# Kernel tuning notes

Hardware: AMD Instinct MI355X
Metric: run time of the kernel (lower is better)

## Reference

```python
import jax, jax.numpy as jnp
import numpy as np

B, D, H = 8192, 256, 64


def setup_inputs() -> dict:
    key = jax.random.key(0)
    ks = jax.random.split(key, 7)
    noise = jax.random.normal(ks[0], (B, D), dtype=jnp.float32)
    adj_logits = jax.random.normal(ks[1], (D, D), dtype=jnp.float32) * 0.1
    # stacked per-node mechanism params: Linear(D,H) -> SiLU -> Linear(H,1)
    W1 = jax.random.normal(ks[2], (D, H, D), dtype=jnp.float32) * (1.0 / np.sqrt(D))
    b1 = jax.random.normal(ks[3], (D, H), dtype=jnp.float32) * (1.0 / np.sqrt(D))
    W2 = jax.random.normal(ks[4], (D, H), dtype=jnp.float32) * (1.0 / np.sqrt(H))
    b2 = jax.random.normal(ks[5], (D,), dtype=jnp.float32) * (1.0 / np.sqrt(H))
    log_sigma = jnp.zeros((D,), dtype=jnp.float32)  # torch init: tensor(0.0)
    return {"noise": noise, "adj_logits": adj_logits, "W1": W1, "b1": b1,
            "W2": W2, "b2": b2, "log_sigma": log_sigma}


def reference(noise, adj_logits, W1, b1, W2, b2, log_sigma):
    d = adj_logits.shape[0]
    # differentiable adjacency: sigmoid(logits) with zeroed diagonal
    adj = jax.nn.sigmoid(adj_logits) * (1.0 - jnp.eye(d, dtype=adj_logits.dtype))
    bsz = noise.shape[0]
    z0 = jnp.zeros((bsz, d), dtype=noise.dtype)

    def step(z, xs):
        i, a_col, w1, bb1, w2, bb2, ls, n_i = xs
        pv = z * a_col[None, :]                       # [B, D] masked parent values
        h = jax.nn.silu(pv @ w1.T + bb1[None, :])     # [B, H]
        det = h @ w2 + bb2                            # [B]
        val = det + jnp.exp(ls) * n_i                 # [B]
        z = jax.lax.dynamic_update_slice(z, val[:, None], (0, i))
        return z, None

    xs = (jnp.arange(d), adj.T, W1, b1, W2, b2, log_sigma, noise.T)
    z, _ = jax.lax.scan(step, z0, xs)
    return z
```

## Files before the change

kernel.cpp:

```cpp
#include <hip/hip_runtime.h>
#include <math.h>

#define Dn 256
#define Hn 64
#define BT 32

typedef __attribute__((ext_vector_type(8))) short short8;
typedef float floatx4 __attribute__((ext_vector_type(4)));

static __device__ __forceinline__ unsigned short f2bf(float x) {
    unsigned int u = __float_as_uint(x);
    unsigned int r = (u + 0x7fffu + ((u >> 16) & 1u)) >> 16;
    return (unsigned short)r;
}

__global__ __launch_bounds__(256) void prep_wb(const float* __restrict__ W1,
                                               const float* __restrict__ adj,
                                               unsigned short* __restrict__ Wb) {
    const int c = blockIdx.x, i = blockIdx.y;
    const int t = threadIdx.x;
    const int w = t >> 6, l = t & 63;
    const int kk = w * 16 + (l & 15);
    const int jb = c * 32 + ((l >> 4) & 3) * 8;
    const float* wp = W1 + ((size_t)i * Hn + kk) * Dn + jb;
    unsigned short v[8];
#pragma unroll
    for (int e = 0; e < 8; ++e) {
        int j = jb + e;
        float m = 0.f;
        if (j != i) m = 1.f / (1.f + __expf(-adj[(size_t)j * Dn + i]));
        v[e] = f2bf(wp[e] * m);
    }
    unsigned short* dst = Wb + ((((size_t)i * 8 + c) * 4 + w) * 64 + l) * 8;
    *(short8*)dst = *(const short8*)v;
}

__global__ __launch_bounds__(256, 1) void scm_main(const unsigned short* __restrict__ Wb,
                                                   const float* __restrict__ b1,
                                                   const float* __restrict__ W2,
                                                   const float* __restrict__ b2,
                                                   const float* __restrict__ log_sigma,
                                                   const float* __restrict__ noise,
                                                   float* __restrict__ out) {
    __shared__ unsigned short zbf[BT][264];
    __shared__ float ns[BT][257];
    __shared__ float part[4][34];
    __shared__ float sgv[Dn];
    __shared__ float b2v[Dn];

    const int t = threadIdx.x;
    const int w = t >> 6;
    const int l = t & 63;
    const int n = l & 15;
    const int q = l >> 4;
    const size_t rowbase = (size_t)blockIdx.x * BT;

    for (int idx = t; idx < BT * 264; idx += 256) (&zbf[0][0])[idx] = 0;
    {
        const float4* np4 = (const float4*)noise;
        for (int idx = t; idx < BT * (Dn / 4); idx += 256) {
            int r = idx >> 6, jq = idx & 63;
            float4 v = np4[(rowbase + r) * (Dn / 4) + jq];
            ns[r][jq * 4 + 0] = v.x; ns[r][jq * 4 + 1] = v.y;
            ns[r][jq * 4 + 2] = v.z; ns[r][jq * 4 + 3] = v.w;
        }
    }
    sgv[t] = __expf(log_sigma[t]);
    b2v[t] = b2[t];
    __syncthreads();

    short8 af0[8], af1[8];
#pragma unroll
    for (int c = 0; c < 8; ++c) { af0[c] = (short8)0; af1[c] = (short8)0; }

    const int kk = w * 16 + n;
    const unsigned short* wb_l = Wb + (size_t)w * 512 + (size_t)l * 8;

    for (int i = 0; i < Dn; ++i) {
        const int cc = (i + 31) >> 5;
        const int lc = (i - 1) >> 5;

        float b1v = b1[i * Hn + kk];
        float w2v = W2[i * Hn + kk];

        short8 bf[8];
        const unsigned short* wrow = wb_l + (size_t)i * 16384;
#pragma unroll
        for (int c = 0; c < 8; ++c)
            if (c < cc) bf[c] = *(const short8*)(wrow + (size_t)c * 2048);

        if (i >= 1) {
#pragma unroll
            for (int c = 0; c < 8; ++c)
                if (c == lc) {
                    af0[c] = *(const short8*)&zbf[n][c * 32 + q * 8];
                    af1[c] = *(const short8*)&zbf[16 + n][c * 32 + q * 8];
                }
        }

        floatx4 acc0 = {0.f, 0.f, 0.f, 0.f};
        floatx4 acc1 = {0.f, 0.f, 0.f, 0.f};
#pragma unroll
        for (int c = 0; c < 8; ++c)
            if (c < cc) {
                acc0 = __builtin_amdgcn_mfma_f32_16x16x32_bf16(af0[c], bf[c], acc0, 0, 0, 0);
                acc1 = __builtin_amdgcn_mfma_f32_16x16x32_bf16(af1[c], bf[c], acc1, 0, 0, 0);
            }

        float d0[4], d1[4];
#pragma unroll
        for (int r = 0; r < 4; ++r) {
            float h0 = acc0[r] + b1v;
            float h1 = acc1[r] + b1v;
            d0[r] = __fdividef(h0, 1.f + __expf(-h0)) * w2v;
            d1[r] = __fdividef(h1, 1.f + __expf(-h1)) * w2v;
        }
#pragma unroll
        for (int m = 1; m <= 8; m <<= 1) {
#pragma unroll
            for (int r = 0; r < 4; ++r) {
                d0[r] += __shfl_xor(d0[r], m);
                d1[r] += __shfl_xor(d1[r], m);
            }
        }
        if (n == 0) {
#pragma unroll
            for (int r = 0; r < 4; ++r) {
                part[w][q * 4 + r]      = d0[r];
                part[w][16 + q * 4 + r] = d1[r];
            }
        }
        __syncthreads();
        if (t < BT) {
            int r = t;
            float z = part[0][r] + part[1][r] + part[2][r] + part[3][r]
                    + b2v[i] + sgv[i] * ns[r][i];
            zbf[r][i] = f2bf(z);
            out[(rowbase + r) * Dn + i] = z;
        }
        __syncthreads();
    }
}

extern "C" void kernel_launch(void* const* d_in, const int* in_sizes, int n_in,
                              void* d_out, int out_size, void* d_ws, size_t ws_size,
                              hipStream_t stream) {
    const float* noise      = (const float*)d_in[0];
    const float* adj_logits = (const float*)d_in[1];
    const float* W1         = (const float*)d_in[2];
    const float* b1         = (const float*)d_in[3];
    const float* W2         = (const float*)d_in[4];
    const float* b2         = (const float*)d_in[5];
    const float* log_sigma  = (const float*)d_in[6];
    float* out = (float*)d_out;

    const int B = in_sizes[0] / Dn;
    unsigned short* Wb = (unsigned short*)d_ws;

    dim3 g1(8, Dn);
    prep_wb<<<g1, 256, 0, stream>>>(W1, adj_logits, Wb);

    dim3 g2(B / BT);
    scm_main<<<g2, 256, 0, stream>>>(Wb, b1, W2, b2, log_sigma, noise, out);
}
```

Baseline: 424.7 us.

## Make each wave own 16 rows and remove block barriers from the sequential scan

```diff
diff --git a/kernel.cpp b/kernel.cpp
--- a/kernel.cpp
+++ b/kernel.cpp
@@ -3,7 +3,6 @@
 
 #define Dn 256
 #define Hn 64
-#define BT 32
 
 typedef __attribute__((ext_vector_type(8))) short short8;
 typedef float floatx4 __attribute__((ext_vector_type(4)));
@@ -14,131 +13,175 @@
     return (unsigned short)r;
 }
 
+__global__ __launch_bounds__(256) void prep_sgm(const float* __restrict__ adj,
+                                                float* __restrict__ sgm) {
+    const int i = blockIdx.x, j = threadIdx.x;
+    float m = 0.f;
+    if (j != i) m = 1.f / (1.f + __expf(-adj[(size_t)j * Dn + i]));
+    sgm[(size_t)i * Dn + j] = m;
+}
+
 __global__ __launch_bounds__(256) void prep_wb(const float* __restrict__ W1,
-                                               const float* __restrict__ adj,
+                                               const float* __restrict__ sgm,
                                                unsigned short* __restrict__ Wb) {
     const int c = blockIdx.x, i = blockIdx.y;
     const int t = threadIdx.x;
-    const int w = t >> 6, l = t & 63;
-    const int kk = w * 16 + (l & 15);
+    const int nb = t >> 6, l = t & 63;
+    const int kk = nb * 16 + (l & 15);
     const int jb = c * 32 + ((l >> 4) & 3) * 8;
     const float* wp = W1 + ((size_t)i * Hn + kk) * Dn + jb;
+    const float* sp = sgm + (size_t)i * Dn + jb;
     unsigned short v[8];
 #pragma unroll
-    for (int e = 0; e < 8; ++e) {
-        int j = jb + e;
-        float m = 0.f;
-        if (j != i) m = 1.f / (1.f + __expf(-adj[(size_t)j * Dn + i]));
-        v[e] = f2bf(wp[e] * m);
-    }
-    unsigned short* dst = Wb + ((((size_t)i * 8 + c) * 4 + w) * 64 + l) * 8;
+    for (int e = 0; e < 8; ++e) v[e] = f2bf(wp[e] * sp[e]);
+    unsigned short* dst = Wb + ((((size_t)i * 8 + c) * 4 + nb) * 64 + l) * 8;
     *(short8*)dst = *(const short8*)v;
 }
 
-__global__ __launch_bounds__(256, 1) void scm_main(const unsigned short* __restrict__ Wb,
+__global__ __launch_bounds__(256) void prep_nst(const float* __restrict__ noise,
+                                                const float* __restrict__ ls,
+                                                float* __restrict__ nsT, int B) {
+    __shared__ float tile[64][65];
+    const int bi = blockIdx.x * 64, dj = blockIdx.y * 64;
+    const int t = threadIdx.x, c = t & 63, rq = t >> 6;
+#pragma unroll
+    for (int it = 0; it < 16; ++it) {
+        int b = bi + it * 4 + rq;
+        tile[it * 4 + rq][c] = noise[(size_t)b * Dn + dj + c];
+    }
+    __syncthreads();
+#pragma unroll
+    for (int it = 0; it < 16; ++it) {
+        int d = dj + it * 4 + rq;
+        float sg = __expf(ls[d]);
+        nsT[(size_t)d * B + bi + c] = tile[c][it * 4 + rq] * sg;
+    }
+}
+
+__global__ __launch_bounds__(128, 1) void scm_main(const unsigned short* __restrict__ Wb,
                                                    const float* __restrict__ b1,
                                                    const float* __restrict__ W2,
                                                    const float* __restrict__ b2,
-                                                   const float* __restrict__ log_sigma,
-                                                   const float* __restrict__ noise,
-                                                   float* __restrict__ out) {
-    __shared__ unsigned short zbf[BT][264];
-    __shared__ float ns[BT][257];
-    __shared__ float part[4][34];
-    __shared__ float sgv[Dn];
-    __shared__ float b2v[Dn];
-
+                                                   const float* __restrict__ nsT,
+                                                   float* __restrict__ out, int B) {
+    __shared__ unsigned short zbf[32][264];
     const int t = threadIdx.x;
-    const int w = t >> 6;
-    const int l = t & 63;
-    const int n = l & 15;
-    const int q = l >> 4;
-    const size_t rowbase = (size_t)blockIdx.x * BT;
-
-    for (int idx = t; idx < BT * 264; idx += 256) (&zbf[0][0])[idx] = 0;
+    const int w = t >> 6, l = t & 63;
+    const int n = l & 15, q = l >> 4;
+    const int rowbase = blockIdx.x * 32 + w * 16;
+
+    for (int idx = l; idx < 16 * 132; idx += 64) {
+        int r = idx / 132, cc = idx - r * 132;
+        ((unsigned int*)zbf[w * 16 + r])[cc] = 0u;
+    }
+
+    const unsigned short* wb_l = Wb + (size_t)l * 8;
+    const unsigned short* zrow_lds = &zbf[w * 16 + n][0];
+
+    short8 af[8];
+    short8 bf[8][4];
+    float b1v[4], w2v[4], b2v;
+    float4 nv;
+
     {
-        const float4* np4 = (const float4*)noise;
-        for (int idx = t; idx < BT * (Dn / 4); idx += 256) {
-            int r = idx >> 6, jq = idx & 63;
-            float4 v = np4[(rowbase + r) * (Dn / 4) + jq];
-            ns[r][jq * 4 + 0] = v.x; ns[r][jq * 4 + 1] = v.y;
-            ns[r][jq * 4 + 2] = v.z; ns[r][jq * 4 + 3] = v.w;
+#pragma unroll
+        for (int nb = 0; nb < 4; ++nb) bf[0][nb] = *(const short8*)(wb_l + nb * 512);
+#pragma unroll
+        for (int nb = 0; nb < 4; ++nb) {
+            b1v[nb] = b1[nb * 16 + n];
+            w2v[nb] = W2[nb * 16 + n];
         }
-    }
-    sgv[t] = __expf(log_sigma[t]);
-    b2v[t] = b2[t];
-    __syncthreads();
-
-    short8 af0[8], af1[8];
-#pragma unroll
-    for (int c = 0; c < 8; ++c) { af0[c] = (short8)0; af1[c] = (short8)0; }
-
-    const int kk = w * 16 + n;
-    const unsigned short* wb_l = Wb + (size_t)w * 512 + (size_t)l * 8;
-
-    for (int i = 0; i < Dn; ++i) {
-        const int cc = (i + 31) >> 5;
-        const int lc = (i - 1) >> 5;
-
-        float b1v = b1[i * Hn + kk];
-        float w2v = W2[i * Hn + kk];
-
-        short8 bf[8];
-        const unsigned short* wrow = wb_l + (size_t)i * 16384;
-#pragma unroll
-        for (int c = 0; c < 8; ++c)
-            if (c < cc) bf[c] = *(const short8*)(wrow + (size_t)c * 2048);
-
-        if (i >= 1) {
+        nv  = *(const float4*)(nsT + rowbase + q * 4);
+        b2v = b2[0];
+    }
+
+#pragma unroll
+    for (int sec = 0; sec < 8; ++sec) {
+        if (sec > 0) {
+            af[sec - 1] = *(const short8*)(zrow_lds + (sec - 1) * 32 + q * 8);
+            const unsigned short* wbp = wb_l + (size_t)(sec * 32) * 16384 + sec * 2048;
+#pragma unroll
+            for (int nb = 0; nb < 4; ++nb) bf[sec][nb] = *(const short8*)(wbp + nb * 512);
+        }
+#pragma unroll 1
+        for (int ii = 0; ii < 32; ++ii) {
+            const int i = sec * 32 + ii;
+
+            short8 ain = *(const short8*)(zrow_lds + sec * 32 + q * 8);
+
+            floatx4 zero4 = {0.f, 0.f, 0.f, 0.f};
+            floatx4 acc[4];
+#pragma unroll
+            for (int nb = 0; nb < 4; ++nb) acc[nb] = zero4;
+
 #pragma unroll
             for (int c = 0; c < 8; ++c)
-                if (c == lc) {
-                    af0[c] = *(const short8*)&zbf[n][c * 32 + q * 8];
-                    af1[c] = *(const short8*)&zbf[16 + n][c * 32 + q * 8];
+                if (c < sec) {
+#pragma unroll
+                    for (int nb = 0; nb < 4; ++nb)
+                        acc[nb] = __builtin_amdgcn_mfma_f32_16x16x32_bf16(af[c], bf[c][nb], acc[nb], 0, 0, 0);
                 }
+#pragma unroll
+            for (int nb = 0; nb < 4; ++nb)
+                acc[nb] = __builtin_amdgcn_mfma_f32_16x16x32_bf16(ain, bf[sec][nb], acc[nb], 0, 0, 0);
+
+            float b1c[4], w2c[4], nvr[4];
+            float b2c = b2v;
+#pragma unroll
+            for (int nb = 0; nb < 4; ++nb) { b1c[nb] = b1v[nb]; w2c[nb] = w2v[nb]; }
+            nvr[0] = nv.x; nvr[1] = nv.y; nvr[2] = nv.z; nvr[3] = nv.w;
+
+            {
+                int ip = i + 1; if (ip > 255) ip = 255;
+                const unsigned short* wbp = wb_l + (size_t)ip * 16384;
+#pragma unroll
+                for (int c = 0; c < 8; ++c)
+                    if (c <= sec) {
+#pragma unroll
+                        for (int nb = 0; nb < 4; ++nb)
+                            bf[c][nb] = *(const short8*)(wbp + c * 2048 + nb * 512);
+                    }
+#pragma unroll
+                for (int nb = 0; nb < 4; ++nb) {
+                    b1v[nb] = b1[ip * Hn + nb * 16 + n];
+                    w2v[nb] = W2[ip * Hn + nb * 16 + n];
+                }
+                nv  = *(const float4*)(nsT + (size_t)ip * B + rowbase + q * 4);
+                b2v = b2[ip];
+            }
+
+            float d[4];
+#pragma unroll
+            for (int r = 0; r < 4; ++r) {
+                float s = 0.f;
+#pragma unroll
+                for (int nb = 0; nb < 4; ++nb) {
+                    float h = acc[nb][r] + b1c[nb];
+                    s += __fdividef(h, 1.f + __expf(-h)) * w2c[nb];
+                }
+                d[r] = s;
+            }
+#pragma unroll
+            for (int m = 1; m <= 8; m <<= 1) {
+#pragma unroll
+                for (int r = 0; r < 4; ++r) d[r] += __shfl_xor(d[r], m);
+            }
+            float z[4];
+#pragma unroll
+            for (int r = 0; r < 4; ++r) z[r] = d[r] + b2c + nvr[r];
+
+            int srcl = ((l & 15) >> 2) << 4;
+            float t0 = __shfl(z[0], srcl), t1 = __shfl(z[1], srcl);
+            float t2 = __shfl(z[2], srcl), t3 = __shfl(z[3], srcl);
+            float za = (l & 1) ? t1 : t0;
+            float zb = (l & 1) ? t3 : t2;
+            float zrow = (l & 2) ? zb : za;
+
+            if (q == 0) {
+                zbf[w * 16 + n][i] = f2bf(zrow);
+                out[(size_t)(rowbase + n) * Dn + i] = zrow;
+            }
         }
-
-        floatx4 acc0 = {0.f, 0.f, 0.f, 0.f};
-        floatx4 acc1 = {0.f, 0.f, 0.f, 0.f};
-#pragma unroll
-        for (int c = 0; c < 8; ++c)
-            if (c < cc) {
-                acc0 = __builtin_amdgcn_mfma_f32_16x16x32_bf16(af0[c], bf[c], acc0, 0, 0, 0);
-                acc1 = __builtin_amdgcn_mfma_f32_16x16x32_bf16(af1[c], bf[c], acc1, 0, 0, 0);
-            }
-
-        float d0[4], d1[4];
-#pragma unroll
-        for (int r = 0; r < 4; ++r) {
-            float h0 = acc0[r] + b1v;
-            float h1 = acc1[r] + b1v;
-            d0[r] = __fdividef(h0, 1.f + __expf(-h0)) * w2v;
-            d1[r] = __fdividef(h1, 1.f + __expf(-h1)) * w2v;
-        }
-#pragma unroll
-        for (int m = 1; m <= 8; m <<= 1) {
-#pragma unroll
-            for (int r = 0; r < 4; ++r) {
-                d0[r] += __shfl_xor(d0[r], m);
-                d1[r] += __shfl_xor(d1[r], m);
-            }
-        }
-        if (n == 0) {
-#pragma unroll
-            for (int r = 0; r < 4; ++r) {
-                part[w][q * 4 + r]      = d0[r];
-                part[w][16 + q * 4 + r] = d1[r];
-            }
-        }
-        __syncthreads();
-        if (t < BT) {
-            int r = t;
-            float z = part[0][r] + part[1][r] + part[2][r] + part[3][r]
-                    + b2v[i] + sgv[i] * ns[r][i];
-            zbf[r][i] = f2bf(z);
-            out[(rowbase + r) * Dn + i] = z;
-        }
-        __syncthreads();
     }
 }
 
@@ -155,11 +198,12 @@
     float* out = (float*)d_out;
 
     const int B = in_sizes[0] / Dn;
-    unsigned short* Wb = (unsigned short*)d_ws;
-
-    dim3 g1(8, Dn);
-    prep_wb<<<g1, 256, 0, stream>>>(W1, adj_logits, Wb);
-
-    dim3 g2(B / BT);
-    scm_main<<<g2, 256, 0, stream>>>(Wb, b1, W2, b2, log_sigma, noise, out);
-}
+    unsigned short* Wb  = (unsigned short*)d_ws;
+    float*          nsT = (float*)((char*)d_ws + (size_t)Dn * Dn * Hn * 2);
+    float*          sgm = nsT;
+
+    prep_sgm<<<dim3(Dn), 256, 0, stream>>>(adj_logits, sgm);
+    prep_wb<<<dim3(8, Dn), 256, 0, stream>>>(W1, sgm, Wb);
+    prep_nst<<<dim3(B / 64, Dn / 64), 256, 0, stream>>>(noise, log_sigma, nsT, B);
+    scm_main<<<dim3(B / 32), 128, 0, stream>>>(Wb, b1, W2, b2, nsT, out, B);
+}
```

New measurement: 382.0 us. 10.1% less time.
